# Performance work log

Measured on AMD Instinct MI355X. Metric: run time of the kernel, lower is better.

Reference implementation:

```python
import jax, jax.numpy as jnp
import numpy as np

BATCH_SIZE = 64
SEQ = 150           # hardcoded 150 in the original module
N = BATCH_SIZE * SEQ  # 9600
D = 128             # feature dim of h_real
K = 16              # n_clusters


def setup_inputs() -> dict:
    key = jax.random.key(0)
    k1, k2 = jax.random.split(key)
    h_real = jax.random.normal(k1, (N, D), dtype=jnp.float32)
    # torch.nn.init.orthogonal_ on an [N, K] tall matrix -> column-orthonormal via QR
    F_raw = jax.random.normal(k2, (N, K), dtype=jnp.float32)
    F, _ = jnp.linalg.qr(F_raw)
    return {"h_real": h_real, "F": F}


def reference(h_real, F):
    # Original: WTW = h h^T (NxN); loss = trace(WTW) - trace(F^T WTW F).
    # Same math without the NxN Gram matrix:
    #   trace(h h^T) = sum(h * h)
    #   trace(F^T h h^T F) = ||h^T F||_F^2
    tr_wtw = jnp.sum(h_real * h_real)
    M = jnp.einsum('nd,nk->dk', h_real, F)  # [D, K]
    tr_fwtwf = jnp.sum(M * M)
    return tr_wtw - tr_fwtwf
```

## Files before the change

### kernel.cpp

```cpp
#include <hip/hip_runtime.h>


#define BLOCKS1  48
#define SSQ_OFF  (BLOCKS1 * 2048)

__global__ __launch_bounds__(1024) void kmeans_part1(
    const float* __restrict__ h, const float* __restrict__ F,
    float* __restrict__ ws, int nrows) {

    const int t   = threadIdx.x;
    const int tm  = t >> 8;
    const int tid = t & 255;
    const int k   = tid & 15;
    const int dg  = tid >> 4;

    const int rpb   = (nrows + BLOCKS1 - 1) / BLOCKS1;
    const int rpt   = (rpb + 3) >> 2;
    const int bbase = blockIdx.x * rpb;
    const int row0  = bbase + tm * rpt;
    int rowend = row0 + rpt;
    if (rowend > bbase + rpb) rowend = bbase + rpb;
    if (rowend > nrows)       rowend = nrows;

    float acc[8] = {0.f,0.f,0.f,0.f,0.f,0.f,0.f,0.f};
    float ssq = 0.f;

    const float4* hb = reinterpret_cast<const float4*>(h);

    #pragma unroll 5
    for (int n = row0; n < rowend; ++n) {
        const float  f = F[(n << 4) + k];
        const float4 a = hb[(n << 5) + (dg << 1) + 0];
        const float4 b = hb[(n << 5) + (dg << 1) + 1];
        acc[0] += a.x * f; acc[1] += a.y * f; acc[2] += a.z * f; acc[3] += a.w * f;
        acc[4] += b.x * f; acc[5] += b.y * f; acc[6] += b.z * f; acc[7] += b.w * f;
        if (k == 0) {
            ssq += a.x * a.x + a.y * a.y + a.z * a.z + a.w * a.w
                 + b.x * b.x + b.y * b.y + b.z * b.z + b.w * b.w;
        }
    }

    __shared__ float part[4][2048];
    __shared__ float ssqp[16];

    #pragma unroll
    for (int j = 0; j < 8; ++j)
        part[tm][(dg << 7) + (((j + dg) & 7) << 4) + k] = acc[j];

    #pragma unroll
    for (int off = 32; off; off >>= 1) ssq += __shfl_down(ssq, off);
    if ((t & 63) == 0) ssqp[t >> 6] = ssq;
    __syncthreads();

    const float2* p2 = reinterpret_cast<const float2*>(part);
    const float2 a2 = p2[         t];
    const float2 b2 = p2[1024  +  t];
    const float2 c2 = p2[2048  +  t];
    const float2 d2 = p2[3072  +  t];
    float2 o;
    o.x = a2.x + b2.x + c2.x + d2.x;
    o.y = a2.y + b2.y + c2.y + d2.y;
    reinterpret_cast<float2*>(ws)[(blockIdx.x << 10) + t] = o;

    if (t == 0) {
        float sq = 0.f;
        #pragma unroll
        for (int i = 0; i < 16; ++i) sq += ssqp[i];
        ws[SSQ_OFF + blockIdx.x] = sq;
    }
}

__global__ __launch_bounds__(512) void kmeans_part2(
    const float* __restrict__ ws, float* __restrict__ out) {

    const int t = threadIdx.x;
    const float4* A = reinterpret_cast<const float4*>(ws);

    float4 m = make_float4(0.f, 0.f, 0.f, 0.f);
    #pragma unroll 8
    for (int b = 0; b < BLOCKS1; ++b) {
        const float4 v = A[(b << 9) + t];
        m.x += v.x; m.y += v.y; m.z += v.z; m.w += v.w;
    }
    float s = m.x * m.x + m.y * m.y + m.z * m.z + m.w * m.w;

    #pragma unroll
    for (int off = 32; off; off >>= 1) s += __shfl_down(s, off);
    __shared__ float red[8];
    if ((t & 63) == 0) red[t >> 6] = s;
    __syncthreads();

    if (t < 64) {
        float v = (t < BLOCKS1) ? ws[SSQ_OFF + t] : 0.f;
        if (t < 8) v -= red[t];
        #pragma unroll
        for (int off = 32; off; off >>= 1) v += __shfl_down(v, off);
        if (t == 0) out[0] = v;
    }
}

extern "C" void kernel_launch(void* const* d_in, const int* in_sizes, int n_in,
                              void* d_out, int out_size, void* d_ws, size_t ws_size,
                              hipStream_t stream) {
    const float* h = (const float*)d_in[0];
    const float* F = (const float*)d_in[1];
    float* out = (float*)d_out;
    float* ws  = (float*)d_ws;

    const int nrows = in_sizes[0] >> 7;

    kmeans_part1<<<BLOCKS1, 1024, 0, stream>>>(h, F, ws, nrows);
    kmeans_part2<<<1, 512, 0, stream>>>(ws, out);
}
```

Baseline: 80.72 us.

## Fuse final reduction into main kernel via last-block atomic counter

Removes the second reduction kernel launch. Each block now bumps a global atomic counter after writing its partials, and the last block to arrive reduces all partials and writes the output. A hipMemsetAsync resets the counter on every call, which adds a small memset operation in place of the removed launch. The final reduction now runs on one 1024-thread block using scalar loads instead of float4 loads.

```diff
diff --git a/kernel.cpp b/kernel.cpp
--- a/kernel.cpp
+++ b/kernel.cpp
@@ -3,10 +3,11 @@
 
 #define BLOCKS1  48
 #define SSQ_OFF  (BLOCKS1 * 2048)
+#define CNT_OFF  (SSQ_OFF + 64)
 
-__global__ __launch_bounds__(1024) void kmeans_part1(
+__global__ __launch_bounds__(1024) void kmeans_fused1(
     const float* __restrict__ h, const float* __restrict__ F,
-    float* __restrict__ ws, int nrows) {
+    float* __restrict__ ws, float* __restrict__ out, int nrows) {
 
     const int t   = threadIdx.x;
     const int tm  = t >> 8;
@@ -52,47 +53,60 @@
     if ((t & 63) == 0) ssqp[t >> 6] = ssq;
     __syncthreads();
 
-    const float2* p2 = reinterpret_cast<const float2*>(part);
-    const float2 a2 = p2[         t];
-    const float2 b2 = p2[1024  +  t];
-    const float2 c2 = p2[2048  +  t];
-    const float2 d2 = p2[3072  +  t];
-    float2 o;
-    o.x = a2.x + b2.x + c2.x + d2.x;
-    o.y = a2.y + b2.y + c2.y + d2.y;
-    reinterpret_cast<float2*>(ws)[(blockIdx.x << 10) + t] = o;
-
+    {
+        const float2* p2 = reinterpret_cast<const float2*>(part);
+        const float2 a2 = p2[         t];
+        const float2 b2 = p2[1024  +  t];
+        const float2 c2 = p2[2048  +  t];
+        const float2 d2 = p2[3072  +  t];
+        float2 o;
+        o.x = a2.x + b2.x + c2.x + d2.x;
+        o.y = a2.y + b2.y + c2.y + d2.y;
+        reinterpret_cast<float2*>(ws)[(blockIdx.x << 10) + t] = o;
+    }
     if (t == 0) {
         float sq = 0.f;
         #pragma unroll
         for (int i = 0; i < 16; ++i) sq += ssqp[i];
         ws[SSQ_OFF + blockIdx.x] = sq;
     }
-}
 
-__global__ __launch_bounds__(512) void kmeans_part2(
-    const float* __restrict__ ws, float* __restrict__ out) {
+    __shared__ bool is_last;
+    __threadfence();
+    __syncthreads();
+    if (t == 0) {
+        unsigned prev = __hip_atomic_fetch_add(
+            reinterpret_cast<unsigned*>(&ws[CNT_OFF]), 1u,
+            __ATOMIC_ACQ_REL, __HIP_MEMORY_SCOPE_AGENT);
+        is_last = (prev == (unsigned)(BLOCKS1 - 1));
+    }
+    __syncthreads();
+    if (!is_last) return;
 
-    const int t = threadIdx.x;
-    const float4* A = reinterpret_cast<const float4*>(ws);
-
-    float4 m = make_float4(0.f, 0.f, 0.f, 0.f);
-    #pragma unroll 8
-    for (int b = 0; b < BLOCKS1; ++b) {
-        const float4 v = A[(b << 9) + t];
-        m.x += v.x; m.y += v.y; m.z += v.z; m.w += v.w;
+    float s = 0.f;
+    #pragma unroll
+    for (int half = 0; half < 2; ++half) {
+        const int c = t + (half << 10);
+        float m = 0.f;
+        #pragma unroll 8
+        for (int b = 0; b < BLOCKS1; ++b) {
+            m += __hip_atomic_load(&ws[(b << 11) + c], __ATOMIC_RELAXED,
+                                   __HIP_MEMORY_SCOPE_AGENT);
+        }
+        s += m * m;
     }
-    float s = m.x * m.x + m.y * m.y + m.z * m.z + m.w * m.w;
-
     #pragma unroll
     for (int off = 32; off; off >>= 1) s += __shfl_down(s, off);
-    __shared__ float red[8];
+    __shared__ float red[16];
     if ((t & 63) == 0) red[t >> 6] = s;
     __syncthreads();
 
     if (t < 64) {
-        float v = (t < BLOCKS1) ? ws[SSQ_OFF + t] : 0.f;
-        if (t < 8) v -= red[t];
+        float v = (t < BLOCKS1)
+            ? __hip_atomic_load(&ws[SSQ_OFF + t], __ATOMIC_RELAXED,
+                                __HIP_MEMORY_SCOPE_AGENT)
+            : 0.f;
+        if (t < 16) v -= red[t];
         #pragma unroll
         for (int off = 32; off; off >>= 1) v += __shfl_down(v, off);
         if (t == 0) out[0] = v;
@@ -109,6 +123,7 @@
 
     const int nrows = in_sizes[0] >> 7;
 
-    kmeans_part1<<<BLOCKS1, 1024, 0, stream>>>(h, F, ws, nrows);
-    kmeans_part2<<<1, 512, 0, stream>>>(ws, out);
+    hipMemsetAsync(ws + CNT_OFF, 0, sizeof(unsigned), stream);
+
+    kmeans_fused1<<<BLOCKS1, 1024, 0, stream>>>(h, F, ws, out, nrows);
 }
```

Measured after the change: 95.94 us. 1.19x slower.
